# Performance work log

Hardware: AMD Instinct MI355X
Metric: run time of the kernel (lower is better)

## Reference

```python
import jax, jax.numpy as jnp
import numpy as np

N, S, P = 262144, 128, 64
LOSS_WEIGHT = 1.0
EPS = np.float32(np.finfo(np.float32).eps)  # lossfun_outer default eps


def setup_inputs() -> dict:
    key = jax.random.key(0)
    k_t, k_w, k_th, k_wh = jax.random.split(key, 4)
    # fine bin edges strictly inside (0,1), sorted along last dim
    t = jnp.sort(jax.random.uniform(k_t, (N, S + 1), minval=1e-4, maxval=1.0 - 1e-4), axis=-1)
    w = jax.random.uniform(k_w, (N, S))
    # proposal bin edges: fixed endpoints 0 and 1 so all t fall inside -> in-range indices
    inner = jnp.sort(jax.random.uniform(k_th, (N, P - 1)), axis=-1)
    t_hat = jnp.concatenate([jnp.zeros((N, 1)), inner, jnp.ones((N, 1))], axis=-1)  # [N, P+1]
    w_hat = jax.random.uniform(k_wh, (N, P))
    return {"t": t, "w": w, "t_hat": t_hat, "w_hat": w_hat}


def _inner_outer(t0, t1, y1):
    # cy1: [N, P+1] prefix sums with leading zero
    cy1 = jnp.concatenate([jnp.zeros_like(y1[..., :1]), jnp.cumsum(y1, axis=-1)], axis=-1)
    # batched binary searches (row-wise sorted t1)
    idx_left = jax.vmap(lambda a, v: jnp.searchsorted(a, v, side='left'))(t1, t0)
    idx_right = jax.vmap(lambda a, v: jnp.searchsorted(a, v, side='right'))(t1, t0)
    cy1_lo = jnp.take_along_axis(cy1, idx_left, axis=-1)   # [N, S+1]
    cy1_hi = jnp.take_along_axis(cy1, idx_right, axis=-1)  # [N, S+1]
    return cy1_hi[..., 1:] - cy1_lo[..., :-1]              # [N, S]


def reference(t, w, t_hat, w_hat):
    w_outer = _inner_outer(t, t_hat, w_hat)
    loss = jnp.maximum(0.0, w - w_outer) ** 2 / (w + EPS)
    return LOSS_WEIGHT * loss  # [N, S], no reduction (matches forward)
```

## Files before the change

kernel.cpp:

```cpp
#include <hip/hip_runtime.h>

namespace {

constexpr int S = 128;
constexpr int P = 64;
constexpr float EPS = 1.1920928955078125e-07f;

__device__ inline float bperm_f(int byteaddr, float v) {
    return __int_as_float(__builtin_amdgcn_ds_bpermute(byteaddr, __float_as_int(v)));
}

__global__ __launch_bounds__(256) void proposal_loss_kernel(
    const float* __restrict__ t,
    const float* __restrict__ w,
    const float* __restrict__ t_hat,
    const float* __restrict__ w_hat,
    float* __restrict__ out)
{
    const int wv   = threadIdx.x >> 6;
    const int lane = threadIdx.x & 63;
    const int row  = (blockIdx.x << 2) + wv;

    const float* t_row  = t     + (size_t)row * (S + 1);
    const float* w_row  = w     + (size_t)row * S;
    const float* th_row = t_hat + (size_t)row * (P + 1);
    const float* wh_row = w_hat + (size_t)row * P;
    float*       o_row  = out   + (size_t)row * S;

    const float th1 = th_row[lane + 1];
    const float wh  = wh_row[lane];
    const float2 tt = *reinterpret_cast<const float2*>(t_row + 2 * lane);
    const float2 ww = *reinterpret_cast<const float2*>(w_row + 2 * lane);
    float tS = 0.0f;
    if (lane == 63) tS = t_row[S];

    float inc = wh;
    #pragma unroll
    for (int d = 1; d < 64; d <<= 1) {
        float o = __shfl_up(inc, d, 64);
        if (lane >= d) inc += o;
    }

    const float t0 = tt.x, t1 = tt.y;
    float t2 = __shfl_down(t0, 1, 64);
    if (lane == 63) t2 = tS;

    auto lb_byte = [&](float v) {
        int posb = 0;
        #pragma unroll
        for (int st = 32; st > 0; st >>= 1) {
            float p = bperm_f(posb + (st - 1) * 4, th1);
            posb += (p < v) ? st * 4 : 0;
        }
        return posb;
    };

    const int b0 = lb_byte(t0);
    const int b1 = lb_byte(t1);
    const int b2 = lb_byte(t2);

    const float q1 = bperm_f(b1, th1);
    const float q2 = bperm_f(b2, th1);
    const int r1b = b1 + ((q1 == t1) ? 4 : 0);
    const int r2b = b2 + ((q2 == t2) ? 4 : 0);

    const float cy_l0 = bperm_f(b0,  inc);
    const float cy_l1 = bperm_f(b1,  inc);
    const float cy_r1 = bperm_f(r1b, inc);
    const float cy_r2 = bperm_f(r2b, inc);

    const float wo0 = cy_r1 - cy_l0;
    const float wo1 = cy_r2 - cy_l1;

    const float d0 = fmaxf(0.0f, ww.x - wo0);
    const float d1 = fmaxf(0.0f, ww.y - wo1);
    float2 res;
    res.x = d0 * d0 * __builtin_amdgcn_rcpf(ww.x + EPS);
    res.y = d1 * d1 * __builtin_amdgcn_rcpf(ww.y + EPS);
    *reinterpret_cast<float2*>(o_row + 2 * lane) = res;
}

}

extern "C" void kernel_launch(void* const* d_in, const int* in_sizes, int n_in,
                              void* d_out, int out_size, void* d_ws, size_t ws_size,
                              hipStream_t stream) {
    const float* t     = (const float*)d_in[0];
    const float* w     = (const float*)d_in[1];
    const float* t_hat = (const float*)d_in[2];
    const float* w_hat = (const float*)d_in[3];
    float* out = (float*)d_out;

    const int N = in_sizes[1] / S;
    proposal_loss_kernel<<<N / 4, 256, 0, stream>>>(t, w, t_hat, w_hat, out);
}
```

Baseline: 100.2 us.

## Use DPP scan and readlane-based top levels for the per-wave binary search

New measurement: 102.1 us. Within noise of the previous version (+1.9%).

```diff
diff --git a/kernel.cpp b/kernel.cpp
--- a/kernel.cpp
+++ b/kernel.cpp
@@ -8,6 +8,17 @@
 
 __device__ inline float bperm_f(int byteaddr, float v) {
     return __int_as_float(__builtin_amdgcn_ds_bpermute(byteaddr, __float_as_int(v)));
+}
+
+template <int CTRL, int ROW_MASK>
+__device__ inline float dpp_add(float v) {
+    int perm = __builtin_amdgcn_update_dpp(0, __float_as_int(v), CTRL, ROW_MASK, 0xf, false);
+    return v + __int_as_float(perm);
+}
+
+template <int LANE>
+__device__ inline float rdlane_f(float v) {
+    return __int_as_float(__builtin_amdgcn_readlane(__float_as_int(v), LANE));
 }
 
 __global__ __launch_bounds__(256) void proposal_loss_kernel(
@@ -27,41 +38,51 @@
     const float* wh_row = w_hat + (size_t)row * P;
     float*       o_row  = out   + (size_t)row * S;
 
-    const float th1 = th_row[lane + 1];
-    const float wh  = wh_row[lane];
-    const float2 tt = *reinterpret_cast<const float2*>(t_row + 2 * lane);
-    const float2 ww = *reinterpret_cast<const float2*>(w_row + 2 * lane);
-    float tS = 0.0f;
-    if (lane == 63) tS = t_row[S];
+    const float  th1 = th_row[lane + 1];
+    const float  wh  = wh_row[lane];
+    const float2 tt  = *reinterpret_cast<const float2*>(t_row + 2 * lane);
+    const float2 ww  = *reinterpret_cast<const float2*>(w_row + 2 * lane);
+    const float  t2  = t_row[2 * lane + 2];
 
     float inc = wh;
-    #pragma unroll
-    for (int d = 1; d < 64; d <<= 1) {
-        float o = __shfl_up(inc, d, 64);
-        if (lane >= d) inc += o;
-    }
+    inc = dpp_add<0x111, 0xf>(inc);
+    inc = dpp_add<0x112, 0xf>(inc);
+    inc = dpp_add<0x114, 0xf>(inc);
+    inc = dpp_add<0x118, 0xf>(inc);
+    inc = dpp_add<0x142, 0xa>(inc);
+    inc = dpp_add<0x143, 0xc>(inc);
 
-    const float t0 = tt.x, t1 = tt.y;
-    float t2 = __shfl_down(t0, 1, 64);
-    if (lane == 63) t2 = tS;
+    const float e31 = rdlane_f<31>(th1);
+    const float e15 = rdlane_f<15>(th1);
+    const float e47 = rdlane_f<47>(th1);
+    const float e7  = rdlane_f<7>(th1);
+    const float e23 = rdlane_f<23>(th1);
+    const float e39 = rdlane_f<39>(th1);
+    const float e55 = rdlane_f<55>(th1);
 
-    auto lb_byte = [&](float v) {
-        int posb = 0;
-        #pragma unroll
-        for (int st = 32; st > 0; st >>= 1) {
-            float p = bperm_f(posb + (st - 1) * 4, th1);
-            posb += (p < v) ? st * 4 : 0;
-        }
+    auto lbb = [&](float v) {
+        int posb = (e31 < v) ? 128 : 0;
+        float l2 = posb ? e47 : e15;
+        posb += (l2 < v) ? 64 : 0;
+        float l3a = (posb & 128) ? e39 : e7;
+        float l3b = (posb & 128) ? e55 : e23;
+        float l3  = (posb & 64) ? l3b : l3a;
+        posb += (l3 < v) ? 32 : 0;
+        float p = bperm_f(posb + 12, th1);  posb += (p < v) ? 16 : 0;
+        p = bperm_f(posb + 4, th1);         posb += (p < v) ? 8 : 0;
+        p = bperm_f(posb, th1);             posb += (p < v) ? 4 : 0;
         return posb;
     };
 
-    const int b0 = lb_byte(t0);
-    const int b1 = lb_byte(t1);
-    const int b2 = lb_byte(t2);
+    const float t0  = tt.x;
+    const float t1v = tt.y;
+    const int b0 = lbb(t0);
+    const int b1 = lbb(t1v);
+    const int b2 = lbb(t2);
 
-    const float q1 = bperm_f(b1, th1);
-    const float q2 = bperm_f(b2, th1);
-    const int r1b = b1 + ((q1 == t1) ? 4 : 0);
+    const float q1 = th_row[(b1 >> 2) + 1];
+    const float q2 = th_row[(b2 >> 2) + 1];
+    const int r1b = b1 + ((q1 == t1v) ? 4 : 0);
     const int r2b = b2 + ((q2 == t2) ? 4 : 0);
 
     const float cy_l0 = bperm_f(b0,  inc);
```
